# Kernel tuning notes

Measured on AMD Instinct MI355X. Metric: run time of the kernel, lower is better.

## Reference

```python
import jax, jax.numpy as jnp
import numpy as np

D_MODEL = 1024
N_HEADS = 16
D_HEAD = D_MODEL // N_HEADS
LN_EPS = 1e-5


def setup_inputs() -> dict:
    key = jax.random.key(0)
    ks = jax.random.split(key, 6)
    s = 1.0 / np.sqrt(D_MODEL)
    x = jax.random.normal(ks[0], (4, 2048, D_MODEL), dtype=jnp.float32)
    w_qkv = jax.random.uniform(ks[1], (3 * D_MODEL, D_MODEL), jnp.float32, -s, s)
    w_out = jax.random.uniform(ks[2], (D_MODEL, D_MODEL), jnp.float32, -s, s)
    w_ffn1 = jax.random.uniform(ks[3], (2 * D_MODEL, D_MODEL), jnp.float32, -s, s)
    w_ffn2 = jax.random.uniform(ks[4], (D_MODEL, 2 * D_MODEL), jnp.float32, -1.0 / np.sqrt(2 * D_MODEL), 1.0 / np.sqrt(2 * D_MODEL))
    return {
        "x": x,
        "w_qkv": w_qkv,
        "w_out": w_out,
        "w_ffn1": w_ffn1,
        "w_ffn2": w_ffn2,
        "g1": jnp.ones((D_MODEL,), jnp.float32),
        "b1": jnp.zeros((D_MODEL,), jnp.float32),
        "g2": jnp.ones((D_MODEL,), jnp.float32),
        "b2": jnp.zeros((D_MODEL,), jnp.float32),
        "temperature": jnp.float32(0.05),
    }


def _layernorm(x, g, b):
    mu = jnp.mean(x, axis=-1, keepdims=True)
    var = jnp.mean(jnp.square(x - mu), axis=-1, keepdims=True)
    return (x - mu) * jax.lax.rsqrt(var + LN_EPS) * g + b


def _l2norm(x, eps=1e-12):
    # matches F.normalize(p=2, dim=-1)
    n = jnp.sqrt(jnp.sum(jnp.square(x), axis=-1, keepdims=True))
    return x / jnp.maximum(n, eps)


def reference(x, w_qkv, w_out, w_ffn1, w_ffn2, g1, b1, g2, b2, temperature):
    B, N, C = x.shape
    residual = x
    h = _layernorm(x, g1, b1)
    qkv = h @ w_qkv.T  # [B,N,3C]
    qkv = qkv.reshape(B, N, 3, N_HEADS, D_HEAD).transpose(2, 0, 3, 1, 4)
    q, k, v = qkv[0], qkv[1], qkv[2]  # each [B,H,N,d]
    qn = _l2norm(q)
    kn = _l2norm(k)
    attn = jnp.einsum('bhnd,bhmd->bhnm', qn, kn) / temperature
    attn = jax.nn.softmax(attn, axis=-1)
    out = jnp.einsum('bhnm,bhmd->bhnd', attn, v)  # [B,H,N,d]
    out = out.transpose(0, 2, 1, 3).reshape(B, N, C)
    x = residual + out @ w_out.T
    residual = x
    h = _layernorm(x, g2, b2)
    h = jax.nn.relu(h @ w_ffn1.T) @ w_ffn2.T
    return residual + h
```

## Files before the change

kernel.cpp:

```cpp
#include <hip/hip_runtime.h>
#include <cstdint>
#include <cstddef>
#include <math.h>

typedef __attribute__((ext_vector_type(8))) short short8;
typedef __attribute__((ext_vector_type(4))) float f32x4;
typedef __attribute__((ext_vector_type(16))) float f32x16;
typedef __attribute__((ext_vector_type(2))) unsigned uint2v;

#define D_MODEL 1024
#define NHEADS 16
#define DHEAD 64
#define BATCH 4
#define SEQ 2048
#define MTOK (BATCH * SEQ)

__device__ __forceinline__ unsigned short f2bf(float f) {
  union { float f; unsigned u; } v; v.f = f;
  unsigned r = v.u + 0x7fffu + ((v.u >> 16) & 1u);
  return (unsigned short)(r >> 16);
}
__device__ __forceinline__ float bf2f(unsigned short u) {
  union { unsigned u; float f; } v; v.u = ((unsigned)u) << 16;
  return v.f;
}
__device__ __forceinline__ unsigned cvt_pk_bf16(float a, float b) {
  unsigned u;
  asm("v_cvt_pk_bf16_f32 %0, %1, %2" : "=v"(u) : "v"(a), "v"(b));
  return u;
}
__device__ __forceinline__ float exp2_fast(float x) {
  float r;
  asm("v_exp_f32 %0, %1" : "=v"(r) : "v"(x));
  return r;
}

typedef const __attribute__((address_space(1))) unsigned int* gas1_t;
typedef __attribute__((address_space(3))) unsigned int* las3_t;
__device__ __forceinline__ void gload16(const unsigned short* g, unsigned short* l) {
  __builtin_amdgcn_global_load_lds((gas1_t)g, (las3_t)l, 16, 0, 0);
}

#define MFMA_BF16(a, b, c) __builtin_amdgcn_mfma_f32_16x16x32_bf16(a, b, c, 0, 0, 0)
#define MFMA32(a, b, c) __builtin_amdgcn_mfma_f32_32x32x16_bf16(a, b, c, 0, 0, 0)

__global__ __launch_bounds__(256) void f32_to_bf16_all(const float* __restrict__ s0,
                                                       const float* __restrict__ s1,
                                                       const float* __restrict__ s2,
                                                       const float* __restrict__ s3,
                                                       unsigned short* __restrict__ d0,
                                                       unsigned short* __restrict__ d1,
                                                       unsigned short* __restrict__ d2,
                                                       unsigned short* __restrict__ d3) {
  int j = blockIdx.x * 256 + threadIdx.x;
  const float* s;
  unsigned short* d;
  if (j < 786432) { s = s0; d = d0; }
  else if ((j -= 786432) < 262144) { s = s1; d = d1; }
  else if ((j -= 262144) < 524288) { s = s2; d = d2; }
  else { j -= 524288; s = s3; d = d3; }
  float4 v = ((const float4*)s)[j];
  ushort4 o;
  o.x = f2bf(v.x); o.y = f2bf(v.y); o.z = f2bf(v.z); o.w = f2bf(v.w);
  ((ushort4*)d)[j] = o;
}

__global__ __launch_bounds__(256) void ln_fwd(const float* __restrict__ x, const float* __restrict__ g,
                                              const float* __restrict__ b,
                                              unsigned short* __restrict__ out) {
  const int row = blockIdx.x, t = threadIdx.x;
  float4 v = *(const float4*)(x + (size_t)row * D_MODEL + t * 4);
  float s = v.x + v.y + v.z + v.w;
  float s2 = v.x * v.x + v.y * v.y + v.z * v.z + v.w * v.w;
#pragma unroll
  for (int m = 1; m < 64; m <<= 1) { s += __shfl_xor(s, m); s2 += __shfl_xor(s2, m); }
  __shared__ float red[8];
  int wv = t >> 6;
  if ((t & 63) == 0) { red[wv] = s; red[4 + wv] = s2; }
  __syncthreads();
  s = red[0] + red[1] + red[2] + red[3];
  s2 = red[4] + red[5] + red[6] + red[7];
  float mu = s * (1.f / D_MODEL);
  float var = s2 * (1.f / D_MODEL) - mu * mu;
  float rs = rsqrtf(var + 1e-5f);
  float4 gg = *(const float4*)(g + t * 4);
  float4 bb = *(const float4*)(b + t * 4);
  ushort4 o;
  o.x = f2bf((v.x - mu) * rs * gg.x + bb.x);
  o.y = f2bf((v.y - mu) * rs * gg.y + bb.y);
  o.z = f2bf((v.z - mu) * rs * gg.z + bb.z);
  o.w = f2bf((v.w - mu) * rs * gg.w + bb.w);
  *(ushort4*)(out + (size_t)row * D_MODEL + t * 4) = o;
}

template <int EPI>
__global__ __launch_bounds__(256) void gemm_bt2(const unsigned short* __restrict__ A,
                                                const unsigned short* __restrict__ B,
                                                const float* __restrict__ R,
                                                const float* __restrict__ Tptr,
                                                void* __restrict__ Cout, int M, int N, int K) {
  constexpr int BM = 128, BN = 128, BK = 32;
  __shared__ unsigned short lA[2][BM * BK], lB[2][BN * BK];
  const int tid = threadIdx.x, lane = tid & 63, wave = tid >> 6;
  const int lo = lane & 15, g = lane >> 4;
  const int nbx = gridDim.x;
  const int o = blockIdx.y * nbx + blockIdx.x;
  const int cpx = (nbx * gridDim.y) >> 3;
  const int w = (o & 7) * cpx + (o >> 3);
  const int bx = w % nbx, by = w / nbx;
  const int bm = by * BM, bn = bx * BN;
  const int wr = wave >> 1, wc = wave & 1;
  f32x4 acc[4][4] = {};
  const int c0 = wave * 128 + lane, c1 = c0 + 64;
  const unsigned short* gA0 = A + (size_t)(bm + (c0 >> 2)) * K + (c0 & 3) * 8;
  const unsigned short* gA1 = A + (size_t)(bm + (c1 >> 2)) * K + (c1 & 3) * 8;
  const unsigned short* gB0 = B + (size_t)(bn + (c0 >> 2)) * K + (c0 & 3) * 8;
  const unsigned short* gB1 = B + (size_t)(bn + (c1 >> 2)) * K + (c1 & 3) * 8;
  const int nk = K / BK;
  auto stage = [&](int buf, int kt) {
    const size_t ko = (size_t)kt * BK;
    gload16(gA0 + ko, &lA[buf][(wave * 128) * 8]);
    gload16(gA1 + ko, &lA[buf][(wave * 128 + 64) * 8]);
    gload16(gB0 + ko, &lB[buf][(wave * 128) * 8]);
    gload16(gB1 + ko, &lB[buf][(wave * 128 + 64) * 8]);
  };
  stage(0, 0);
  for (int kt = 0; kt < nk; ++kt) {
    __syncthreads();
    if (kt + 1 < nk) stage((kt + 1) & 1, kt + 1);
    const unsigned short* La = &lA[kt & 1][0];
    const unsigned short* Lb = &lB[kt & 1][0];
    short8 af[4], bfr[4];
#pragma unroll
    for (int m = 0; m < 4; ++m)
      af[m] = *(const short8*)(La + (wr * 64 + m * 16 + lo) * BK + g * 8);
#pragma unroll
    for (int n = 0; n < 4; ++n)
      bfr[n] = *(const short8*)(Lb + (wc * 64 + n * 16 + lo) * BK + g * 8);
#pragma unroll
    for (int m = 0; m < 4; ++m)
#pragma unroll
      for (int n = 0; n < 4; ++n) acc[m][n] = MFMA_BF16(af[m], bfr[n], acc[m][n]);
  }
  const int r0 = bm + wr * 64 + g * 4;
  const int c0c = bn + wc * 64 + lo;
  if (EPI == 3) {
    const int hb = bn + wc * 64;
    const bool isq = hb < 1024, isk = (hb >= 1024) && (hb < 2048);
    const float qs = 1.44269504088896f / Tptr[0];
#pragma unroll
    for (int m = 0; m < 4; ++m)
#pragma unroll
      for (int r = 0; r < 4; ++r) {
        float sc = 1.0f;
        if (isq || isk) {
          float ss = 0.f;
#pragma unroll
          for (int n = 0; n < 4; ++n) ss += acc[m][n][r] * acc[m][n][r];
          ss += __shfl_xor(ss, 1);
          ss += __shfl_xor(ss, 2);
          ss += __shfl_xor(ss, 4);
          ss += __shfl_xor(ss, 8);
          sc = 1.0f / fmaxf(sqrtf(ss), 1e-12f);
          if (isq) sc *= qs;
        }
#pragma unroll
        for (int n = 0; n < 4; ++n) {
          size_t off = (size_t)(r0 + m * 16 + r) * N + (c0c + n * 16);
          ((unsigned short*)Cout)[off] = f2bf(acc[m][n][r] * sc);
        }
      }
  } else {
#pragma unroll
    for (int m = 0; m < 4; ++m)
#pragma unroll
      for (int n = 0; n < 4; ++n) {
#pragma unroll
        for (int r = 0; r < 4; ++r) {
          size_t off = (size_t)(r0 + m * 16 + r) * N + (c0c + n * 16);
          float v = acc[m][n][r];
          if (EPI == 0) ((unsigned short*)Cout)[off] = f2bf(v);
          else if (EPI == 1) ((float*)Cout)[off] = R[off] + v;
          else ((unsigned short*)Cout)[off] = f2bf(fmaxf(v, 0.f));
        }
      }
  }
}

__global__ __launch_bounds__(256) void transpose_v(const unsigned short* __restrict__ qkv,
                                                   unsigned short* __restrict__ vt) {
  __shared__ unsigned short tile[64][80];
  const int blk = blockIdx.x;
  const int ntile = blk & 31, h = (blk >> 5) & 15, b = blk >> 9;
  const int t = threadIdx.x;
  const int tt = t >> 2, c4 = t & 3;
  size_t rowbase = (size_t)(b * SEQ + ntile * 64 + tt) * 3072 + h * 64 + c4 * 16;
  const unsigned short* pv = qkv + rowbase + 2048;
  *(short8*)&tile[tt][c4 * 16] = *(const short8*)pv;
  *(short8*)&tile[tt][c4 * 16 + 8] = *(const short8*)(pv + 8);
  __syncthreads();
  const int d = tt;
  short8 o0, o1;
#pragma unroll
  for (int j = 0; j < 8; ++j) o0[j] = (short)tile[c4 * 16 + j][d];
#pragma unroll
  for (int j = 0; j < 8; ++j) o1[j] = (short)tile[c4 * 16 + 8 + j][d];
  size_t vr = (size_t)((b * NHEADS + h) * DHEAD + d) * SEQ + ntile * 64 + c4 * 16;
  *(short8*)(vt + vr) = o0;
  *(short8*)(vt + vr + 8) = o1;
}

__global__ __launch_bounds__(256) void attn_fwd9(const unsigned short* __restrict__ qkv,
                                                 const unsigned short* __restrict__ vt,
                                                 unsigned short* __restrict__ out,
                                                 const float* __restrict__ temp) {
  __shared__ unsigned short lK[2][64 * 64];
  __shared__ unsigned short lV[2][64 * 64];
  const int blk = blockIdx.x;
  const int bh = blk & 63, qt = blk >> 6;
  const int b = bh >> 4, h = bh & 15;
  const int tid = threadIdx.x, lane = tid & 63, wave = tid >> 6;
  const int l5 = lane >> 5, l31 = lane & 31;
  const int qr0 = qt * 128 + wave * 32;
  const float M0 = 1.05f * 1.44269504088896f / temp[0];
  f32x16 minit;
#pragma unroll
  for (int r = 0; r < 16; ++r) minit[r] = -M0;
  const unsigned short* qrow = qkv + (size_t)(b * SEQ + qr0 + l31) * 3072 + h * 64 + l5 * 8;
  short8 qf[4];
#pragma unroll
  for (int t = 0; t < 4; ++t) qf[t] = *(const short8*)(qrow + t * 16);
  const int srow = tid >> 3, slot = tid & 7;
  const int sw0 = ((slot ^ (srow & 7)) * 8);
  const unsigned short* gK = qkv + (size_t)(b * SEQ + srow) * 3072 + 1024 + h * 64 + slot * 8;
  const unsigned short* gV = vt + ((size_t)(bh * 64) + srow) * SEQ + slot * 8;
  short8 rk0 = *(const short8*)gK;
  short8 rk1 = *(const short8*)(gK + (size_t)32 * 3072);
  short8 rv0 = *(const short8*)gV;
  short8 rv1 = *(const short8*)(gV + (size_t)32 * SEQ);
  *(short8*)&lK[0][srow * 64 + sw0] = rk0;
  *(short8*)&lK[0][(srow + 32) * 64 + sw0] = rk1;
  *(short8*)&lV[0][srow * 64 + sw0] = rv0;
  *(short8*)&lV[0][(srow + 32) * 64 + sw0] = rv1;
  f32x16 o0 = {}, o1 = {};
  float lsum = 0.f;
  constexpr int NT = SEQ / 64;
  for (int t = 0; t < NT; ++t) {
    __syncthreads();
    const unsigned short* Kb = &lK[t & 1][0];
    const unsigned short* Vb = &lV[t & 1][0];
    if (t + 1 < NT) {
      rk0 = *(const short8*)(gK + (size_t)(t + 1) * 64 * 3072);
      rk1 = *(const short8*)(gK + (size_t)((t + 1) * 64 + 32) * 3072);
      rv0 = *(const short8*)(gV + (t + 1) * 64);
      rv1 = *(const short8*)(gV + (size_t)32 * SEQ + (t + 1) * 64);
    }
#pragma unroll
    for (int tile = 0; tile < 2; ++tile) {
      f32x16 s = minit;
      __builtin_amdgcn_s_setprio(1);
#pragma unroll
      for (int td = 0; td < 4; ++td) {
        const int row = tile * 32 + l31;
        const int sl = ((2 * td + l5) ^ (row & 7)) * 8;
        short8 kf = *(const short8*)(Kb + row * 64 + sl);
        s = MFMA32(kf, qf[td], s);
      }
      __builtin_amdgcn_s_setprio(0);
      float p[16];
#pragma unroll
      for (int r = 0; r < 16; ++r) p[r] = exp2_fast(s[r]);
      float q01 = p[0] + p[1], q23 = p[2] + p[3], q45 = p[4] + p[5], q67 = p[6] + p[7];
      float q89 = p[8] + p[9], qab = p[10] + p[11], qcd = p[12] + p[13], qef = p[14] + p[15];
      float h0 = (q01 + q23) + (q45 + q67);
      float h1 = (q89 + qab) + (qcd + qef);
      lsum += h0 + h1;
      unsigned a0 = cvt_pk_bf16(p[0], p[1]), a1 = cvt_pk_bf16(p[2], p[3]);
      unsigned a2 = cvt_pk_bf16(p[4], p[5]), a3 = cvt_pk_bf16(p[6], p[7]);
      unsigned c0 = cvt_pk_bf16(p[8], p[9]), c1 = cvt_pk_bf16(p[10], p[11]);
      unsigned c2 = cvt_pk_bf16(p[12], p[13]), c3 = cvt_pk_bf16(p[14], p[15]);
      uint2v w0 = __builtin_amdgcn_permlane32_swap(a0, a2, false, false);
      uint2v w1 = __builtin_amdgcn_permlane32_swap(a1, a3, false, false);
      uint2v w2 = __builtin_amdgcn_permlane32_swap(c0, c2, false, false);
      uint2v w3 = __builtin_amdgcn_permlane32_swap(c1, c3, false, false);
      union { unsigned u[4]; short8 v; } f0, f1;
      f0.u[0] = w0.x; f0.u[1] = w1.x; f0.u[2] = w0.y; f0.u[3] = w1.y;
      f1.u[0] = w2.x; f1.u[1] = w3.x; f1.u[2] = w2.y; f1.u[3] = w3.y;
      __builtin_amdgcn_s_setprio(1);
      {
        const int vrow0 = l31, vrow1 = 32 + l31;
        const int sa = ((2 * (tile * 2) + l5) ^ (vrow0 & 7)) * 8;
        const int sb = ((2 * (tile * 2 + 1) + l5) ^ (vrow0 & 7)) * 8;
        short8 va0 = *(const short8*)(Vb + vrow0 * 64 + sa);
        short8 vb0 = *(const short8*)(Vb + vrow0 * 64 + sb);
        short8 va1 = *(const short8*)(Vb + vrow1 * 64 + sa);
        short8 vb1 = *(const short8*)(Vb + vrow1 * 64 + sb);
        o0 = MFMA32(va0, f0.v, o0);
        o0 = MFMA32(vb0, f1.v, o0);
        o1 = MFMA32(va1, f0.v, o1);
        o1 = MFMA32(vb1, f1.v, o1);
      }
      __builtin_amdgcn_s_setprio(0);
    }
    if (t + 1 < NT) {
      *(short8*)&lK[(t + 1) & 1][srow * 64 + sw0] = rk0;
      *(short8*)&lK[(t + 1) & 1][(srow + 32) * 64 + sw0] = rk1;
      *(short8*)&lV[(t + 1) & 1][srow * 64 + sw0] = rv0;
      *(short8*)&lV[(t + 1) & 1][(srow + 32) * 64 + sw0] = rv1;
    }
  }
  lsum += __shfl_xor(lsum, 32);
  const float rinv = 1.0f / lsum;
  unsigned short* orow = out + (size_t)(b * SEQ + qr0 + l31) * D_MODEL + h * 64 + l5 * 4;
#pragma unroll
  for (int rq = 0; rq < 4; ++rq)
#pragma unroll
    for (int rr = 0; rr < 4; rr += 2) {
      *(unsigned*)(orow + rq * 8 + rr) =
          cvt_pk_bf16(o0[rq * 4 + rr] * rinv, o0[rq * 4 + rr + 1] * rinv);
      *(unsigned*)(orow + 32 + rq * 8 + rr) =
          cvt_pk_bf16(o1[rq * 4 + rr] * rinv, o1[rq * 4 + rr + 1] * rinv);
    }
}

extern "C" void kernel_launch(void* const* d_in, const int* in_sizes, int n_in, void* d_out,
                              int out_size, void* d_ws, size_t ws_size, hipStream_t stream) {
  const float* x = (const float*)d_in[0];
  const float* w_qkv = (const float*)d_in[1];
  const float* w_out = (const float*)d_in[2];
  const float* w_ffn1 = (const float*)d_in[3];
  const float* w_ffn2 = (const float*)d_in[4];
  const float* g1 = (const float*)d_in[5];
  const float* b1 = (const float*)d_in[6];
  const float* g2 = (const float*)d_in[7];
  const float* b2 = (const float*)d_in[8];
  const float* temp = (const float*)d_in[9];
  float* outp = (float*)d_out;

  char* ws = (char*)d_ws;
  size_t off = 0;
  auto alloc = [&](size_t bytes) {
    void* p = ws + off;
    off += (bytes + 255) & ~(size_t)255;
    return p;
  };
  unsigned short* wqkv_bf = (unsigned short*)alloc((size_t)3072 * 1024 * 2);
  unsigned short* wout_bf = (unsigned short*)alloc((size_t)1024 * 1024 * 2);
  unsigned short* wf1_bf = (unsigned short*)alloc((size_t)2048 * 1024 * 2);
  unsigned short* wf2_bf = (unsigned short*)alloc((size_t)1024 * 2048 * 2);
  unsigned short* h_bf = (unsigned short*)alloc((size_t)MTOK * 1024 * 2);
  unsigned short* qkv_bf = (unsigned short*)alloc((size_t)MTOK * 3072 * 2);
  unsigned short* vt_bf = (unsigned short*)alloc((size_t)BATCH * NHEADS * DHEAD * SEQ * 2);
  unsigned short* ao_bf = (unsigned short*)alloc((size_t)MTOK * 1024 * 2);
  float* x2 = (float*)alloc((size_t)MTOK * 1024 * 4);

  f32_to_bf16_all<<<8192, 256, 0, stream>>>(w_qkv, w_out, w_ffn1, w_ffn2, wqkv_bf, wout_bf, wf1_bf,
                                            wf2_bf);
  ln_fwd<<<MTOK, 256, 0, stream>>>(x, g1, b1, h_bf);
  gemm_bt2<3><<<dim3(3072 / 128, MTOK / 128), 256, 0, stream>>>(h_bf, wqkv_bf, nullptr, temp,
                                                                (void*)qkv_bf, MTOK, 3072, 1024);
  transpose_v<<<BATCH * NHEADS * (SEQ / 64), 256, 0, stream>>>(qkv_bf, vt_bf);
  attn_fwd9<<<BATCH * NHEADS * (SEQ / 128), 256, 0, stream>>>(qkv_bf, vt_bf, ao_bf, temp);
  gemm_bt2<1><<<dim3(1024 / 128, MTOK / 128), 256, 0, stream>>>(ao_bf, wout_bf, x, nullptr,
                                                                (void*)x2, MTOK, 1024, 1024);
  ln_fwd<<<MTOK, 256, 0, stream>>>(x2, g2, b2, h_bf);
  gemm_bt2<2><<<dim3(2048 / 128, MTOK / 128), 256, 0, stream>>>(h_bf, wf1_bf, nullptr, nullptr,
                                                                (void*)qkv_bf, MTOK, 2048, 1024);
  gemm_bt2<1><<<dim3(1024 / 128, MTOK / 128), 256, 0, stream>>>(qkv_bf, wf2_bf, x2, nullptr,
                                                                (void*)outp, MTOK, 1024, 2048);
}
```

Measured before the change: 325.5 us.

## Replace GEMM with 256x128 triple-buffered 32x32 MFMA kernel using swizzled LDS

The GEMM kernel is rewritten with 512 threads, a 256x128 block tile and BK=64. It uses 32x32x16 MFMA instead of 16x16x32, XOR-swizzled LDS layout and a three-stage global_load_lds pipeline whose loads are interleaved between MFMA groups with explicit barriers and priority hints. The aim is more reuse per loaded byte, fewer LDS bank conflicts and better overlap of memory with compute. In exchange it uses more LDS (144KB) and has many barriers per K step, which may limit occupancy. Grids for the small-N GEMMs also halve in block count.

```diff
diff --git a/kernel.cpp b/kernel.cpp
--- a/kernel.cpp
+++ b/kernel.cpp
@@ -41,7 +41,6 @@
   __builtin_amdgcn_global_load_lds((gas1_t)g, (las3_t)l, 16, 0, 0);
 }
 
-#define MFMA_BF16(a, b, c) __builtin_amdgcn_mfma_f32_16x16x32_bf16(a, b, c, 0, 0, 0)
 #define MFMA32(a, b, c) __builtin_amdgcn_mfma_f32_32x32x16_bf16(a, b, c, 0, 0, 0)
 
 __global__ __launch_bounds__(256) void f32_to_bf16_all(const float* __restrict__ s0,
@@ -94,96 +93,172 @@
 }
 
 template <int EPI>
-__global__ __launch_bounds__(256) void gemm_bt2(const unsigned short* __restrict__ A,
+__global__ __launch_bounds__(512) void gemm_bt3(const unsigned short* __restrict__ A,
                                                 const unsigned short* __restrict__ B,
                                                 const float* __restrict__ R,
                                                 const float* __restrict__ Tptr,
                                                 void* __restrict__ Cout, int M, int N, int K) {
-  constexpr int BM = 128, BN = 128, BK = 32;
-  __shared__ unsigned short lA[2][BM * BK], lB[2][BN * BK];
+  constexpr int BM = 256, BN = 128, BK = 64;
+  __shared__ unsigned short lA[3][BM * BK];
+  __shared__ unsigned short lB[3][BN * BK];
   const int tid = threadIdx.x, lane = tid & 63, wave = tid >> 6;
-  const int lo = lane & 15, g = lane >> 4;
+  const int l31 = lane & 31, l5 = lane >> 5;
+  const int wm = wave >> 1, wn = wave & 1;
   const int nbx = gridDim.x;
   const int o = blockIdx.y * nbx + blockIdx.x;
   const int cpx = (nbx * gridDim.y) >> 3;
   const int w = (o & 7) * cpx + (o >> 3);
   const int bx = w % nbx, by = w / nbx;
   const int bm = by * BM, bn = bx * BN;
-  const int wr = wave >> 1, wc = wave & 1;
-  f32x4 acc[4][4] = {};
-  const int c0 = wave * 128 + lane, c1 = c0 + 64;
-  const unsigned short* gA0 = A + (size_t)(bm + (c0 >> 2)) * K + (c0 & 3) * 8;
-  const unsigned short* gA1 = A + (size_t)(bm + (c1 >> 2)) * K + (c1 & 3) * 8;
-  const unsigned short* gB0 = B + (size_t)(bn + (c0 >> 2)) * K + (c0 & 3) * 8;
-  const unsigned short* gB1 = B + (size_t)(bn + (c1 >> 2)) * K + (c1 & 3) * 8;
-  const int nk = K / BK;
-  auto stage = [&](int buf, int kt) {
-    const size_t ko = (size_t)kt * BK;
-    gload16(gA0 + ko, &lA[buf][(wave * 128) * 8]);
-    gload16(gA1 + ko, &lA[buf][(wave * 128 + 64) * 8]);
-    gload16(gB0 + ko, &lB[buf][(wave * 128) * 8]);
-    gload16(gB1 + ko, &lB[buf][(wave * 128 + 64) * 8]);
-  };
-  stage(0, 0);
-  for (int kt = 0; kt < nk; ++kt) {
-    __syncthreads();
-    if (kt + 1 < nk) stage((kt + 1) & 1, kt + 1);
-    const unsigned short* La = &lA[kt & 1][0];
-    const unsigned short* Lb = &lB[kt & 1][0];
-    short8 af[4], bfr[4];
-#pragma unroll
-    for (int m = 0; m < 4; ++m)
-      af[m] = *(const short8*)(La + (wr * 64 + m * 16 + lo) * BK + g * 8);
-#pragma unroll
-    for (int n = 0; n < 4; ++n)
-      bfr[n] = *(const short8*)(Lb + (wc * 64 + n * 16 + lo) * BK + g * 8);
-#pragma unroll
-    for (int m = 0; m < 4; ++m)
-#pragma unroll
-      for (int n = 0; n < 4; ++n) acc[m][n] = MFMA_BF16(af[m], bfr[n], acc[m][n]);
+  const int srow8 = lane >> 3;
+  const int sslot = (lane & 7) ^ srow8;
+  const unsigned short* sA0 = A + (size_t)(bm + wave * 8 + srow8) * K + sslot * 8;
+  const unsigned short* sA1 = sA0 + (size_t)64 * K;
+  const unsigned short* sA2 = sA0 + (size_t)128 * K;
+  const unsigned short* sA3 = sA0 + (size_t)192 * K;
+  const unsigned short* sB0 = B + (size_t)(bn + wave * 8 + srow8) * K + sslot * 8;
+  const unsigned short* sB1 = sB0 + (size_t)64 * K;
+  const int sx = l31 & 7;
+  const int ar0 = (wm * 64 + l31) * 64, ar1 = ar0 + 32 * 64;
+  const int br0 = (wn * 64 + l31) * 64, br1 = br0 + 32 * 64;
+  const int k0 = ((0 + l5) ^ sx) * 8, k1 = ((2 + l5) ^ sx) * 8;
+  const int k2 = ((4 + l5) ^ sx) * 8, k3 = ((6 + l5) ^ sx) * 8;
+  f32x16 acc00 = {}, acc01 = {}, acc10 = {}, acc11 = {};
+  const int NK = K / BK;
+  {
+    gload16(sA0, &lA[0][(wave * 8) * 64]);
+    gload16(sA1, &lA[0][(64 + wave * 8) * 64]);
+    gload16(sA2, &lA[0][(128 + wave * 8) * 64]);
+    gload16(sA3, &lA[0][(192 + wave * 8) * 64]);
+    gload16(sB0, &lB[0][(wave * 8) * 64]);
+    gload16(sB1, &lB[0][(64 + wave * 8) * 64]);
+    gload16(sA0 + 64, &lA[1][(wave * 8) * 64]);
+    gload16(sA1 + 64, &lA[1][(64 + wave * 8) * 64]);
+    gload16(sA2 + 64, &lA[1][(128 + wave * 8) * 64]);
+    gload16(sA3 + 64, &lA[1][(192 + wave * 8) * 64]);
+    gload16(sB0 + 64, &lB[1][(wave * 8) * 64]);
+    gload16(sB1 + 64, &lB[1][(64 + wave * 8) * 64]);
+    asm volatile("s_waitcnt vmcnt(6)" ::: "memory");
+    asm volatile("s_barrier" ::: "memory");
   }
-  const int r0 = bm + wr * 64 + g * 4;
-  const int c0c = bn + wc * 64 + lo;
+  for (int t = 0; t < NK; ++t) {
+    const unsigned short* La = &lA[t % 3][0];
+    const unsigned short* Lb = &lB[t % 3][0];
+    const int bufn = (t + 2) % 3;
+    const bool pre = (t + 2 < NK);
+    const size_t ko = (size_t)(t + 2) * 64;
+    {
+      short8 a0 = *(const short8*)(La + ar0 + k0), a1 = *(const short8*)(La + ar0 + k1);
+      short8 a2 = *(const short8*)(La + ar0 + k2), a3 = *(const short8*)(La + ar0 + k3);
+      short8 b0 = *(const short8*)(Lb + br0 + k0), b1 = *(const short8*)(Lb + br0 + k1);
+      short8 b2 = *(const short8*)(Lb + br0 + k2), b3 = *(const short8*)(Lb + br0 + k3);
+      if (pre) {
+        gload16(sA0 + ko, &lA[bufn][(wave * 8) * 64]);
+        gload16(sA1 + ko, &lA[bufn][(64 + wave * 8) * 64]);
+      }
+      asm volatile("s_barrier" ::: "memory");
+      __builtin_amdgcn_s_setprio(1);
+      acc00 = MFMA32(a0, b0, acc00); acc00 = MFMA32(a1, b1, acc00);
+      acc00 = MFMA32(a2, b2, acc00); acc00 = MFMA32(a3, b3, acc00);
+      __builtin_amdgcn_s_setprio(0);
+      asm volatile("s_barrier" ::: "memory");
+    }
+    {
+      short8 a0 = *(const short8*)(La + ar0 + k0), a1 = *(const short8*)(La + ar0 + k1);
+      short8 a2 = *(const short8*)(La + ar0 + k2), a3 = *(const short8*)(La + ar0 + k3);
+      short8 b0 = *(const short8*)(Lb + br1 + k0), b1 = *(const short8*)(Lb + br1 + k1);
+      short8 b2 = *(const short8*)(Lb + br1 + k2), b3 = *(const short8*)(Lb + br1 + k3);
+      if (pre) {
+        gload16(sA2 + ko, &lA[bufn][(128 + wave * 8) * 64]);
+        gload16(sA3 + ko, &lA[bufn][(192 + wave * 8) * 64]);
+      }
+      asm volatile("s_barrier" ::: "memory");
+      __builtin_amdgcn_s_setprio(1);
+      acc01 = MFMA32(a0, b0, acc01); acc01 = MFMA32(a1, b1, acc01);
+      acc01 = MFMA32(a2, b2, acc01); acc01 = MFMA32(a3, b3, acc01);
+      __builtin_amdgcn_s_setprio(0);
+      asm volatile("s_barrier" ::: "memory");
+    }
+    {
+      short8 a0 = *(const short8*)(La + ar1 + k0), a1 = *(const short8*)(La + ar1 + k1);
+      short8 a2 = *(const short8*)(La + ar1 + k2), a3 = *(const short8*)(La + ar1 + k3);
+      short8 b0 = *(const short8*)(Lb + br0 + k0), b1 = *(const short8*)(Lb + br0 + k1);
+      short8 b2 = *(const short8*)(Lb + br0 + k2), b3 = *(const short8*)(Lb + br0 + k3);
+      if (pre) gload16(sB0 + ko, &lB[bufn][(wave * 8) * 64]);
+      asm volatile("s_barrier" ::: "memory");
+      __builtin_amdgcn_s_setprio(1);
+      acc10 = MFMA32(a0, b0, acc10); acc10 = MFMA32(a1, b1, acc10);
+      acc10 = MFMA32(a2, b2, acc10); acc10 = MFMA32(a3, b3, acc10);
+      __builtin_amdgcn_s_setprio(0);
+      asm volatile("s_barrier" ::: "memory");
+    }
+    {
+      short8 a0 = *(const short8*)(La + ar1 + k0), a1 = *(const short8*)(La + ar1 + k1);
+      short8 a2 = *(const short8*)(La + ar1 + k2), a3 = *(const short8*)(La + ar1 + k3);
+      short8 b0 = *(const short8*)(Lb + br1 + k0), b1 = *(const short8*)(Lb + br1 + k1);
+      short8 b2 = *(const short8*)(Lb + br1 + k2), b3 = *(const short8*)(Lb + br1 + k3);
+      if (pre) gload16(sB1 + ko, &lB[bufn][(64 + wave * 8) * 64]);
+      asm volatile("s_barrier" ::: "memory");
+      __builtin_amdgcn_s_setprio(1);
+      acc11 = MFMA32(a0, b0, acc11); acc11 = MFMA32(a1, b1, acc11);
+      acc11 = MFMA32(a2, b2, acc11); acc11 = MFMA32(a3, b3, acc11);
+      __builtin_amdgcn_s_setprio(0);
+      if (pre) asm volatile("s_waitcnt vmcnt(6)" ::: "memory");
+      else if (t + 1 < NK) asm volatile("s_waitcnt vmcnt(0)" ::: "memory");
+      asm volatile("s_barrier" ::: "memory");
+    }
+  }
+  const int r0 = bm + wm * 64 + 4 * l5;
+  const int c0 = bn + wn * 64;
   if (EPI == 3) {
-    const int hb = bn + wc * 64;
-    const bool isq = hb < 1024, isk = (hb >= 1024) && (hb < 2048);
+    const bool isq = c0 < 1024, isk = (c0 >= 1024) && (c0 < 2048);
     const float qs = 1.44269504088896f / Tptr[0];
 #pragma unroll
-    for (int m = 0; m < 4; ++m)
-#pragma unroll
-      for (int r = 0; r < 4; ++r) {
+    for (int i = 0; i < 2; ++i) {
+      const f32x16 va = (i == 0) ? acc00 : acc10;
+      const f32x16 vb = (i == 0) ? acc01 : acc11;
+#pragma unroll
+      for (int reg = 0; reg < 16; ++reg) {
+        float a0 = va[reg], a1 = vb[reg];
         float sc = 1.0f;
         if (isq || isk) {
-          float ss = 0.f;
-#pragma unroll
-          for (int n = 0; n < 4; ++n) ss += acc[m][n][r] * acc[m][n][r];
+          float ss = a0 * a0 + a1 * a1;
           ss += __shfl_xor(ss, 1);
           ss += __shfl_xor(ss, 2);
           ss += __shfl_xor(ss, 4);
           ss += __shfl_xor(ss, 8);
+          ss += __shfl_xor(ss, 16);
           sc = 1.0f / fmaxf(sqrtf(ss), 1e-12f);
           if (isq) sc *= qs;
         }
-#pragma unroll
-        for (int n = 0; n < 4; ++n) {
-          size_t off = (size_t)(r0 + m * 16 + r) * N + (c0c + n * 16);
-          ((unsigned short*)Cout)[off] = f2bf(acc[m][n][r] * sc);
+        const int row = r0 + i * 32 + (reg & 3) + 8 * (reg >> 2);
+        ((unsigned short*)Cout)[(size_t)row * N + (c0 + l31)] = f2bf(a0 * sc);
+        ((unsigned short*)Cout)[(size_t)row * N + (c0 + 32 + l31)] = f2bf(a1 * sc);
+      }
+    }
+  } else {
+#pragma unroll
+    for (int i = 0; i < 2; ++i) {
+      const f32x16 va = (i == 0) ? acc00 : acc10;
+      const f32x16 vb = (i == 0) ? acc01 : acc11;
+#pragma unroll
+      for (int reg = 0; reg < 16; ++reg) {
+        const int row = r0 + i * 32 + (reg & 3) + 8 * (reg >> 2);
+        size_t off0 = (size_t)row * N + (c0 + l31);
+        size_t off1 = (size_t)row * N + (c0 + 32 + l31);
+        float v0 = va[reg], v1 = vb[reg];
+        if (EPI == 0) {
+          ((unsigned short*)Cout)[off0] = f2bf(v0);
+          ((unsigned short*)Cout)[off1] = f2bf(v1);
+        } else if (EPI == 1) {
+          ((float*)Cout)[off0] = R[off0] + v0;
+          ((float*)Cout)[off1] = R[off1] + v1;
+        } else {
+          ((unsigned short*)Cout)[off0] = f2bf(fmaxf(v0, 0.f));
+          ((unsigned short*)Cout)[off1] = f2bf(fmaxf(v1, 0.f));
         }
       }
-  } else {
-#pragma unroll
-    for (int m = 0; m < 4; ++m)
-#pragma unroll
-      for (int n = 0; n < 4; ++n) {
-#pragma unroll
-        for (int r = 0; r < 4; ++r) {
-          size_t off = (size_t)(r0 + m * 16 + r) * N + (c0c + n * 16);
-          float v = acc[m][n][r];
-          if (EPI == 0) ((unsigned short*)Cout)[off] = f2bf(v);
-          else if (EPI == 1) ((float*)Cout)[off] = R[off] + v;
-          else ((unsigned short*)Cout)[off] = f2bf(fmaxf(v, 0.f));
-        }
-      }
+    }
   }
 }
 
@@ -272,9 +347,7 @@
       for (int r = 0; r < 16; ++r) p[r] = exp2_fast(s[r]);
       float q01 = p[0] + p[1], q23 = p[2] + p[3], q45 = p[4] + p[5], q67 = p[6] + p[7];
       float q89 = p[8] + p[9], qab = p[10] + p[11], qcd = p[12] + p[13], qef = p[14] + p[15];
-      float h0 = (q01 + q23) + (q45 + q67);
-      float h1 = (q89 + qab) + (qcd + qef);
-      lsum += h0 + h1;
+      lsum += ((q01 + q23) + (q45 + q67)) + ((q89 + qab) + (qcd + qef));
       unsigned a0 = cvt_pk_bf16(p[0], p[1]), a1 = cvt_pk_bf16(p[2], p[3]);
       unsigned a2 = cvt_pk_bf16(p[4], p[5]), a3 = cvt_pk_bf16(p[6], p[7]);
       unsigned c0 = cvt_pk_bf16(p[8], p[9]), c1 = cvt_pk_bf16(p[10], p[11]);
@@ -357,15 +430,15 @@
   f32_to_bf16_all<<<8192, 256, 0, stream>>>(w_qkv, w_out, w_ffn1, w_ffn2, wqkv_bf, wout_bf, wf1_bf,
                                             wf2_bf);
   ln_fwd<<<MTOK, 256, 0, stream>>>(x, g1, b1, h_bf);
-  gemm_bt2<3><<<dim3(3072 / 128, MTOK / 128), 256, 0, stream>>>(h_bf, wqkv_bf, nullptr, temp,
+  gemm_bt3<3><<<dim3(3072 / 128, MTOK / 256), 512, 0, stream>>>(h_bf, wqkv_bf, nullptr, temp,
                                                                 (void*)qkv_bf, MTOK, 3072, 1024);
   transpose_v<<<BATCH * NHEADS * (SEQ / 64), 256, 0, stream>>>(qkv_bf, vt_bf);
   attn_fwd9<<<BATCH * NHEADS * (SEQ / 128), 256, 0, stream>>>(qkv_bf, vt_bf, ao_bf, temp);
-  gemm_bt2<1><<<dim3(1024 / 128, MTOK / 128), 256, 0, stream>>>(ao_bf, wout_bf, x, nullptr,
+  gemm_bt3<1><<<dim3(1024 / 128, MTOK / 256), 512, 0, stream>>>(ao_bf, wout_bf, x, nullptr,
                                                                 (void*)x2, MTOK, 1024, 1024);
   ln_fwd<<<MTOK, 256, 0, stream>>>(x2, g2, b2, h_bf);
-  gemm_bt2<2><<<dim3(2048 / 128, MTOK / 128), 256, 0, stream>>>(h_bf, wf1_bf, nullptr, nullptr,
+  gemm_bt3<2><<<dim3(2048 / 128, MTOK / 256), 512, 0, stream>>>(h_bf, wf1_bf, nullptr, nullptr,
                                                                 (void*)qkv_bf, MTOK, 2048, 1024);
-  gemm_bt2<1><<<dim3(1024 / 128, MTOK / 128), 256, 0, stream>>>(qkv_bf, wf2_bf, x2, nullptr,
+  gemm_bt3<1><<<dim3(1024 / 128, MTOK / 256), 512, 0, stream>>>(qkv_bf, wf2_bf, x2, nullptr,
                                                                 (void*)outp, MTOK, 1024, 2048);
 }
```

Result: slower. 389.2 us (+19.6%).
